# Kernel optimization log

Measured on AMD Instinct MI355X. Metric: run time of the kernel, lower is better.

Reference implementation:

```python
import jax, jax.numpy as jnp
import numpy as np

SCALING_FACTOR = 128.0


def setup_inputs() -> dict:
    key = jax.random.key(0)
    k1, k2, k3, k4 = jax.random.split(key, 4)
    B, G1, G2, DX, DZ, NT = 4, 128, 128, 2, 128, 2048
    x_grid = jax.random.uniform(k1, (B, G1, G2, DX), dtype=jnp.float32)
    z_grid = jax.random.normal(k2, (B, G1, G2, DZ), dtype=jnp.float32)
    xt = jax.random.uniform(k3, (B, NT, DX), dtype=jnp.float32)
    # raw (pre-softplus) lengthscale parameter, one per input dim
    init_ls = 0.1
    lengthscale_param = jnp.full((DX,), np.log(np.exp(init_ls) - 1.0), dtype=jnp.float32)
    lengthscale_param = lengthscale_param + 0.01 * jax.random.normal(k4, (DX,), dtype=jnp.float32)
    return {"x_grid": x_grid, "z_grid": z_grid, "xt": xt, "lengthscale_param": lengthscale_param}


def reference(x_grid, z_grid, xt, lengthscale_param):
    B = x_grid.shape[0]
    dx = x_grid.shape[-1]
    dz = z_grid.shape[-1]
    # flatten spatial grid dims -> (B, ng, d)
    xg = x_grid.reshape(B, -1, dx)
    zg = z_grid.reshape(B, -1, dz)
    # lengthscale = 1e-5 + softplus(param), shape (dx,)
    ls = 1e-5 + jax.nn.softplus(lengthscale_param)
    # pairwise scaled squared distances: (B, nt, ng)
    diff = (xt[:, :, None, :] - xg[:, None, :, :]) / ls  # (B, nt, ng, dx)
    dist2 = jnp.sum(diff * diff, axis=-1)
    weights = jnp.exp(-0.5 * dist2)  # (B, nt, ng)
    # weighted smoothing onto targets
    out = jnp.einsum("btg,bgz->btz", weights, zg) / SCALING_FACTOR
    return out
```

## Files before the change

kernel.cpp:

```cpp
#include <hip/hip_runtime.h>
#include <hip/hip_bf16.h>
#include <cstdint>
#include <cstddef>


typedef float  f32x4  __attribute__((ext_vector_type(4)));
typedef float  f32x16 __attribute__((ext_vector_type(16)));
typedef short  short8 __attribute__((ext_vector_type(8)));
typedef unsigned short ushort4v __attribute__((ext_vector_type(4)));
typedef unsigned short ushort8 __attribute__((ext_vector_type(8)));

#if __has_builtin(__builtin_amdgcn_exp2f)
#define EXP2F(x) __builtin_amdgcn_exp2f(x)
#else
#define EXP2F(x) exp2f(x)
#endif

#define AS1C(p) ((const __attribute__((address_space(1))) void*)(p))
#define AS3(p)  ((__attribute__((address_space(3))) void*)(p))

__device__ __forceinline__ unsigned short bf16_bits(float f) {
  __bf16 h = (__bf16)f;
  return __builtin_bit_cast(unsigned short, h);
}

__global__ __launch_bounds__(256) void pre_kernel(
    const float* __restrict__ x_grid, const float* __restrict__ z_grid,
    const float* __restrict__ xt, const float* __restrict__ lsp,
    unsigned short* __restrict__ zgb, float* __restrict__ xg_trip,
    float* __restrict__ xt4)
{
  __shared__ unsigned short lt[64 * 128];
  const int bid = blockIdx.x;
  const int b   = bid >> 8;
  const int grp = bid & 255;
  const int tid = threadIdx.x;
  const size_t gbase = (size_t)b * 16384 + grp * 64;
  const float sc = 1.0f / 128.0f;

  const float* zr = z_grid + gbase * 128;
  #pragma unroll
  for (int it = 0; it < 8; ++it) {
    const int idx = it * 256 + tid;
    const int row = idx >> 5, c4 = idx & 31;
    f32x4 v = *(const f32x4*)(zr + row * 128 + c4 * 4);
    ushort4v o;
    o.x = bf16_bits(v.x * sc); o.y = bf16_bits(v.y * sc);
    o.z = bf16_bits(v.z * sc); o.w = bf16_bits(v.w * sc);
    *(ushort4v*)(lt + row * 128 + c4 * 4) = o;
  }

  if (tid < 128) {
    const float ls0 = 1e-5f + log1pf(expf(lsp[0]));
    const float ls1 = 1e-5f + log1pf(expf(lsp[1]));
    const float cs  = sqrtf(0.7213475204444817f);
    const float s0 = cs / ls0, s1 = cs / ls1;
    if (tid < 64) {
      const size_t g = gbase + tid;
      const float u0 = x_grid[g * 2 + 0] * s0;
      const float u1 = x_grid[g * 2 + 1] * s1;
      float* d = xg_trip + g * 3;
      d[0] = 2.0f * u0; d[1] = 2.0f * u1; d[2] = -(u0 * u0 + u1 * u1);
    } else if (bid < 128) {
      const int bx = bid >> 5;
      const int r  = (bid & 31) * 64 + (tid - 64);
      const float u0 = xt[((size_t)(bx * 2048 + r)) * 2 + 0] * s0;
      const float u1 = xt[((size_t)(bx * 2048 + r)) * 2 + 1] * s1;
      f32x4 d; d.x = u0; d.y = u1; d.z = -(u0 * u0 + u1 * u1); d.w = 0.0f;
      *(f32x4*)(xt4 + ((size_t)(bx * 2048 + r)) * 4) = d;
    }
  }

  __syncthreads();

  const int q2p = tid >> 7, c = tid & 127;
  #pragma unroll
  for (int h = 0; h < 4; ++h) {
    ushort8 o;
    #pragma unroll
    for (int hi = 0; hi < 2; ++hi)
      #pragma unroll
      for (int j = 0; j < 4; ++j)
        o[hi * 4 + j] = lt[(h * 16 + 4 * q2p + 8 * hi + j) * 128 + c];
    *(ushort8*)(zgb + ((size_t)(b * 1024 + grp * 4 + h)) * 2048
                    + (size_t)(q2p * 128 + c) * 8) = o;
  }
}

__global__ __launch_bounds__(128, 2) void main_kernel(
    const unsigned short* __restrict__ zgb,
    const float* __restrict__ xg_trip,
    const float* __restrict__ xt4,
    float* __restrict__ out)
{
  __shared__ __align__(128) char smem[12288 + 12288];
  char* ring = smem;
  char* trip = smem + 12288;

  const int raw = blockIdx.x;
  const int lid = (raw & 7) * 128 + (raw >> 3);
  const int mt  = lid & 15;
  const int b   = (lid >> 4) & 3;
  const int ksp = lid >> 6;

  const int tid = threadIdx.x;
  const int rh  = tid >> 6;
  const int l   = tid & 63;
  const int l31 = l & 31;
  const int q2  = l >> 5;

  float at0[2], at1[2], ca[2];
  #pragma unroll
  for (int mi = 0; mi < 2; ++mi) {
    const int r = mt * 128 + rh * 64 + mi * 32 + l31;
    f32x4 v = *(const f32x4*)(xt4 + ((size_t)(b * 2048 + r)) * 4);
    at0[mi] = v.x; at1[mi] = v.y; ca[mi] = v.z;
  }

  f32x16 acc[2][4];
  #pragma unroll
  for (int mi = 0; mi < 2; ++mi)
    #pragma unroll
    for (int ni = 0; ni < 4; ++ni)
      #pragma unroll
      for (int e = 0; e < 16; ++e)
        acc[mi][ni][e] = 0.0f;

  const char* zsrc = (const char*)zgb + ((size_t)(b * 1024 + ksp * 64)) * 4096;
  const char* tsrc = (const char*)xg_trip + ((size_t)(b * 16384 + ksp * 1024)) * 12;

  auto stage = [&](int s) {
    const char* zs = zsrc + (size_t)s * 4096 + rh * 2048;
    char* zd = ring + (s % 3) * 4096 + rh * 2048;
    __builtin_amdgcn_global_load_lds(AS1C(zs + l * 16), AS3(zd + l * 16), 16, 0, 0);
    __builtin_amdgcn_global_load_lds(AS1C(zs + 1024 + l * 16),
                                     AS3(zd + 1024 + l * 16), 16, 0, 0);
  };

  #pragma unroll
  for (int w = 0; w < 6; ++w) {
    const int off = (rh * 6 + w) * 1024 + l * 16;
    __builtin_amdgcn_global_load_lds(AS1C(tsrc + off), AS3(trip + off), 16, 0, 0);
  }
  stage(0);
  stage(1);

  for (int s = 0; s < 64; ++s) {
    if (s < 63) { asm volatile("s_waitcnt vmcnt(2)" ::: "memory"); }
    else        { asm volatile("s_waitcnt vmcnt(0)" ::: "memory"); }
    __builtin_amdgcn_s_barrier();
    asm volatile("" ::: "memory");

    if (s + 2 < 64) stage(s + 2);

    const float* tb = (const float*)(trip + s * 192 + q2 * 48);
    f32x4 L0 = *(const f32x4*)(tb + 0);
    f32x4 L1 = *(const f32x4*)(tb + 4);
    f32x4 L2 = *(const f32x4*)(tb + 8);
    f32x4 H0 = *(const f32x4*)(tb + 24);
    f32x4 H1 = *(const f32x4*)(tb + 28);
    f32x4 H2 = *(const f32x4*)(tb + 32);
    float g0[8], g1[8], cb[8];
    g0[0]=L0.x; g1[0]=L0.y; cb[0]=L0.z;
    g0[1]=L0.w; g1[1]=L1.x; cb[1]=L1.y;
    g0[2]=L1.z; g1[2]=L1.w; cb[2]=L2.x;
    g0[3]=L2.y; g1[3]=L2.z; cb[3]=L2.w;
    g0[4]=H0.x; g1[4]=H0.y; cb[4]=H0.z;
    g0[5]=H0.w; g1[5]=H1.x; cb[5]=H1.y;
    g0[6]=H1.z; g1[6]=H1.w; cb[6]=H2.x;
    g0[7]=H2.y; g1[7]=H2.z; cb[7]=H2.w;

    const char* zt = ring + (s % 3) * 4096 + q2 * 2048 + l31 * 16;
    short8 bfr[4];
    #pragma unroll
    for (int ni = 0; ni < 4; ++ni)
      bfr[ni] = *(const short8*)(zt + ni * 512);

    short8 af[2];
    #pragma unroll
    for (int mi = 0; mi < 2; ++mi) {
      union { short8 s8; __bf16 e[8]; } u;
      #pragma unroll
      for (int j = 0; j < 8; ++j) {
        float arg = __builtin_fmaf(at0[mi], g0[j],
                    __builtin_fmaf(at1[mi], g1[j], ca[mi] + cb[j]));
        u.e[j] = (__bf16)EXP2F(arg);
      }
      af[mi] = u.s8;
    }

    #pragma unroll
    for (int mi = 0; mi < 2; ++mi)
      #pragma unroll
      for (int ni = 0; ni < 4; ++ni)
        acc[mi][ni] = __builtin_amdgcn_mfma_f32_32x32x16_bf16(
            af[mi], bfr[ni], acc[mi][ni], 0, 0, 0);
  }

  #pragma unroll
  for (int mi = 0; mi < 2; ++mi)
    #pragma unroll
    for (int ni = 0; ni < 4; ++ni)
      #pragma unroll
      for (int r = 0; r < 16; ++r) {
        const int row = mt * 128 + rh * 64 + mi * 32
                      + (r & 3) + 8 * (r >> 2) + 4 * q2;
        atomicAdd(out + ((size_t)b * 2048 + row) * 128 + ni * 32 + l31,
                  acc[mi][ni][r]);
      }
}

extern "C" void kernel_launch(void* const* d_in, const int* in_sizes, int n_in,
                              void* d_out, int out_size, void* d_ws, size_t ws_size,
                              hipStream_t stream) {
  const float* x_grid = (const float*)d_in[0];
  const float* z_grid = (const float*)d_in[1];
  const float* xt     = (const float*)d_in[2];
  const float* lsp    = (const float*)d_in[3];
  float* out = (float*)d_out;

  char* ws = (char*)d_ws;
  unsigned short* zgb = (unsigned short*)ws;
  float* xg_trip = (float*)(ws + 16777216);
  float* xt4     = (float*)(ws + 16777216 + 786432);

  hipMemsetAsync(d_out, 0, (size_t)out_size * sizeof(float), stream);
  pre_kernel<<<1024, 256, 0, stream>>>(x_grid, z_grid, xt, lsp,
                                       zgb, xg_trip, xt4);
  main_kernel<<<1024, 128, 0, stream>>>(zgb, xg_trip, xt4, out);
}
```

Baseline: 171.0 us.

## Split K across wave pairs with LDS reduction and replace atomics by partial-sum reduce

Each main_kernel block now has 256 threads: two wave pairs work on adjacent K chunks and combine their accumulators through LDS, which halves the grid to 512 blocks. When the workspace is large enough, the final per-K-split results go as plain stores into a partials buffer, and a new reduce_kernel sums the 8 splits. This replaces the memset plus fp32 atomics to the output. The cost is a larger 64KB LDS footprint per block, extra syncs, and a third kernel launch that reads 32MB of partials.

```diff
diff --git a/kernel.cpp b/kernel.cpp
--- a/kernel.cpp
+++ b/kernel.cpp
@@ -87,27 +87,31 @@
   }
 }
 
-__global__ __launch_bounds__(128, 2) void main_kernel(
+__global__ __launch_bounds__(256, 2) void main_kernel(
     const unsigned short* __restrict__ zgb,
     const float* __restrict__ xg_trip,
     const float* __restrict__ xt4,
-    float* __restrict__ out)
+    float* __restrict__ out,
+    float* __restrict__ partials)
 {
-  __shared__ __align__(128) char smem[12288 + 12288];
+  __shared__ __align__(128) char smem[65536];
   char* ring = smem;
-  char* trip = smem + 12288;
+  char* trip = smem + 24576;
 
   const int raw = blockIdx.x;
-  const int lid = (raw & 7) * 128 + (raw >> 3);
+  const int lid = (raw & 7) * 64 + (raw >> 3);
   const int mt  = lid & 15;
   const int b   = (lid >> 4) & 3;
   const int ksp = lid >> 6;
 
   const int tid = threadIdx.x;
-  const int rh  = tid >> 6;
+  const int wv  = tid >> 6;
   const int l   = tid & 63;
+  const int rh  = wv & 1;
+  const int kk  = wv >> 1;
   const int l31 = l & 31;
   const int q2  = l >> 5;
+  const int chunk = ksp * 2 + kk;
 
   float at0[2], at1[2], ca[2];
   #pragma unroll
@@ -126,12 +130,12 @@
       for (int e = 0; e < 16; ++e)
         acc[mi][ni][e] = 0.0f;
 
-  const char* zsrc = (const char*)zgb + ((size_t)(b * 1024 + ksp * 64)) * 4096;
-  const char* tsrc = (const char*)xg_trip + ((size_t)(b * 16384 + ksp * 1024)) * 12;
+  const char* zsrc = (const char*)zgb + ((size_t)(b * 1024 + chunk * 64)) * 4096;
+  const char* tsrc = (const char*)xg_trip + ((size_t)(b * 16384 + ksp * 2048)) * 12;
 
   auto stage = [&](int s) {
     const char* zs = zsrc + (size_t)s * 4096 + rh * 2048;
-    char* zd = ring + (s % 3) * 4096 + rh * 2048;
+    char* zd = ring + (s % 3) * 8192 + kk * 4096 + rh * 2048;
     __builtin_amdgcn_global_load_lds(AS1C(zs + l * 16), AS3(zd + l * 16), 16, 0, 0);
     __builtin_amdgcn_global_load_lds(AS1C(zs + 1024 + l * 16),
                                      AS3(zd + 1024 + l * 16), 16, 0, 0);
@@ -139,12 +143,13 @@
 
   #pragma unroll
   for (int w = 0; w < 6; ++w) {
-    const int off = (rh * 6 + w) * 1024 + l * 16;
+    const int off = wv * 6144 + w * 1024 + l * 16;
     __builtin_amdgcn_global_load_lds(AS1C(tsrc + off), AS3(trip + off), 16, 0, 0);
   }
   stage(0);
   stage(1);
 
+  #pragma unroll 3
   for (int s = 0; s < 64; ++s) {
     if (s < 63) { asm volatile("s_waitcnt vmcnt(2)" ::: "memory"); }
     else        { asm volatile("s_waitcnt vmcnt(0)" ::: "memory"); }
@@ -153,7 +158,7 @@
 
     if (s + 2 < 64) stage(s + 2);
 
-    const float* tb = (const float*)(trip + s * 192 + q2 * 48);
+    const float* tb = (const float*)(trip + kk * 12288 + s * 192 + q2 * 48);
     f32x4 L0 = *(const f32x4*)(tb + 0);
     f32x4 L1 = *(const f32x4*)(tb + 4);
     f32x4 L2 = *(const f32x4*)(tb + 8);
@@ -170,7 +175,7 @@
     g0[6]=H1.z; g1[6]=H1.w; cb[6]=H2.x;
     g0[7]=H2.y; g1[7]=H2.z; cb[7]=H2.w;
 
-    const char* zt = ring + (s % 3) * 4096 + q2 * 2048 + l31 * 16;
+    const char* zt = ring + (s % 3) * 8192 + kk * 4096 + q2 * 2048 + l31 * 16;
     short8 bfr[4];
     #pragma unroll
     for (int ni = 0; ni < 4; ++ni)
@@ -197,17 +202,63 @@
             af[mi], bfr[ni], acc[mi][ni], 0, 0, 0);
   }
 
-  #pragma unroll
-  for (int mi = 0; mi < 2; ++mi)
-    #pragma unroll
-    for (int ni = 0; ni < 4; ++ni)
-      #pragma unroll
-      for (int r = 0; r < 16; ++r) {
-        const int row = mt * 128 + rh * 64 + mi * 32
-                      + (r & 3) + 8 * (r >> 2) + 4 * q2;
-        atomicAdd(out + ((size_t)b * 2048 + row) * 128 + ni * 32 + l31,
-                  acc[mi][ni][r]);
+  __syncthreads();
+  if (kk == 1) {
+    #pragma unroll
+    for (int mi = 0; mi < 2; ++mi)
+      #pragma unroll
+      for (int ni = 0; ni < 4; ++ni)
+        #pragma unroll
+        for (int q = 0; q < 4; ++q) {
+          f32x4 v;
+          v.x = acc[mi][ni][q * 4 + 0]; v.y = acc[mi][ni][q * 4 + 1];
+          v.z = acc[mi][ni][q * 4 + 2]; v.w = acc[mi][ni][q * 4 + 3];
+          *(f32x4*)(smem + rh * 32768 + (mi * 4 + ni) * 4096 + q * 1024 + l * 16) = v;
+        }
+  }
+  __syncthreads();
+  if (kk == 0) {
+    float* pb = partials ? partials + ((size_t)(ksp * 64 + b * 16 + mt)) * 16384
+                         : nullptr;
+    #pragma unroll
+    for (int mi = 0; mi < 2; ++mi)
+      #pragma unroll
+      for (int ni = 0; ni < 4; ++ni) {
+        #pragma unroll
+        for (int q = 0; q < 4; ++q) {
+          f32x4 v = *(const f32x4*)(smem + rh * 32768 + (mi * 4 + ni) * 4096
+                                         + q * 1024 + l * 16);
+          acc[mi][ni][q * 4 + 0] += v.x; acc[mi][ni][q * 4 + 1] += v.y;
+          acc[mi][ni][q * 4 + 2] += v.z; acc[mi][ni][q * 4 + 3] += v.w;
+        }
+        #pragma unroll
+        for (int r = 0; r < 16; ++r) {
+          const int row = rh * 64 + mi * 32
+                        + (r & 3) + 8 * (r >> 2) + 4 * q2;
+          const int col = ni * 32 + l31;
+          if (pb) {
+            pb[row * 128 + col] = acc[mi][ni][r];
+          } else {
+            atomicAdd(out + ((size_t)b * 2048 + mt * 128 + row) * 128 + col,
+                      acc[mi][ni][r]);
+          }
+        }
       }
+  }
+}
+
+__global__ __launch_bounds__(256) void reduce_kernel(
+    const float* __restrict__ partials, float* __restrict__ out)
+{
+  const size_t base = ((size_t)blockIdx.x * 256 + threadIdx.x) * 4;
+  const float* p = partials + base;
+  f32x4 s = *(const f32x4*)p;
+  #pragma unroll
+  for (int ksv = 1; ksv < 8; ++ksv) {
+    f32x4 v = *(const f32x4*)(p + (size_t)ksv * 1048576);
+    s.x += v.x; s.y += v.y; s.z += v.z; s.w += v.w;
+  }
+  *(f32x4*)(out + base) = s;
 }
 
 extern "C" void kernel_launch(void* const* d_in, const int* in_sizes, int n_in,
@@ -223,9 +274,15 @@
   unsigned short* zgb = (unsigned short*)ws;
   float* xg_trip = (float*)(ws + 16777216);
   float* xt4     = (float*)(ws + 16777216 + 786432);
-
-  hipMemsetAsync(d_out, 0, (size_t)out_size * sizeof(float), stream);
+  const size_t poff = 16777216 + 786432 + 131072;
+  const bool use_partials = ws_size >= poff + 33554432;
+  float* partials = use_partials ? (float*)(ws + poff) : nullptr;
+
+  if (!use_partials)
+    hipMemsetAsync(d_out, 0, (size_t)out_size * sizeof(float), stream);
   pre_kernel<<<1024, 256, 0, stream>>>(x_grid, z_grid, xt, lsp,
                                        zgb, xg_trip, xt4);
-  main_kernel<<<1024, 128, 0, stream>>>(zgb, xg_trip, xt4, out);
-}
+  main_kernel<<<512, 256, 0, stream>>>(zgb, xg_trip, xt4, out, partials);
+  if (use_partials)
+    reduce_kernel<<<1024, 256, 0, stream>>>(partials, out);
+}
```

New measurement: 140.8 us. -17.7%, faster.

## Shrink main-kernel tiles, deepen pipeline, replace atomics with partial-sum reduction

Applied to the files above, without the earlier changes.

Each main-kernel block now covers 64 target rows instead of 128 and 8 K-splits instead of 16. Each warp holds a single 32-row MFMA tile, which cuts registers enough to raise the occupancy hint to 4 blocks per SIMD. The grid triplets are streamed through a 4-slot LDS ring with prefetch depth 3 instead of being preloaded, shrinking LDS use. When workspace allows, per-K-split results go to a partials buffer and a separate reduce kernel sums them, replacing the memset and float atomics. The trade-off is twice as many exp evaluations per B-fragment load, extra global traffic for the partials, and an added launch.

```diff
diff --git a/kernel.cpp b/kernel.cpp
--- a/kernel.cpp
+++ b/kernel.cpp
@@ -87,73 +87,71 @@
   }
 }
 
-__global__ __launch_bounds__(128, 2) void main_kernel(
+__global__ __launch_bounds__(128, 4) void main_kernel(
     const unsigned short* __restrict__ zgb,
     const float* __restrict__ xg_trip,
     const float* __restrict__ xt4,
-    float* __restrict__ out)
+    float* __restrict__ out,
+    float* __restrict__ partials)
 {
-  __shared__ __align__(128) char smem[12288 + 12288];
+  __shared__ __align__(128) char smem[4 * 4096 + 4 * 256];
   char* ring = smem;
-  char* trip = smem + 12288;
+  char* trg  = smem + 16384;
 
   const int raw = blockIdx.x;
   const int lid = (raw & 7) * 128 + (raw >> 3);
-  const int mt  = lid & 15;
-  const int b   = (lid >> 4) & 3;
-  const int ksp = lid >> 6;
+  const int mt  = lid & 31;
+  const int b   = (lid >> 5) & 3;
+  const int ksp = lid >> 7;
 
   const int tid = threadIdx.x;
-  const int rh  = tid >> 6;
+  const int w   = tid >> 6;
   const int l   = tid & 63;
   const int l31 = l & 31;
   const int q2  = l >> 5;
 
-  float at0[2], at1[2], ca[2];
-  #pragma unroll
-  for (int mi = 0; mi < 2; ++mi) {
-    const int r = mt * 128 + rh * 64 + mi * 32 + l31;
-    f32x4 v = *(const f32x4*)(xt4 + ((size_t)(b * 2048 + r)) * 4);
-    at0[mi] = v.x; at1[mi] = v.y; ca[mi] = v.z;
-  }
-
-  f32x16 acc[2][4];
-  #pragma unroll
-  for (int mi = 0; mi < 2; ++mi)
-    #pragma unroll
-    for (int ni = 0; ni < 4; ++ni)
-      #pragma unroll
-      for (int e = 0; e < 16; ++e)
-        acc[mi][ni][e] = 0.0f;
-
-  const char* zsrc = (const char*)zgb + ((size_t)(b * 1024 + ksp * 64)) * 4096;
-  const char* tsrc = (const char*)xg_trip + ((size_t)(b * 16384 + ksp * 1024)) * 12;
+  const int r = mt * 64 + w * 32 + l31;
+  f32x4 tv = *(const f32x4*)(xt4 + ((size_t)(b * 2048 + r)) * 4);
+  const float at0 = tv.x, at1 = tv.y, ca = tv.z;
+
+  f32x16 acc[4];
+  #pragma unroll
+  for (int ni = 0; ni < 4; ++ni)
+    #pragma unroll
+    for (int e = 0; e < 16; ++e)
+      acc[ni][e] = 0.0f;
+
+  const char* zsrc = (const char*)zgb + ((size_t)(b * 1024 + ksp * 128)) * 4096;
+  const char* tsrc = (const char*)xg_trip + ((size_t)(b * 16384 + ksp * 2048)) * 12;
 
   auto stage = [&](int s) {
-    const char* zs = zsrc + (size_t)s * 4096 + rh * 2048;
-    char* zd = ring + (s % 3) * 4096 + rh * 2048;
+    const int sl = s & 3;
+    const char* zs = zsrc + (size_t)s * 4096 + w * 2048;
+    char* zd = ring + sl * 4096 + w * 2048;
     __builtin_amdgcn_global_load_lds(AS1C(zs + l * 16), AS3(zd + l * 16), 16, 0, 0);
     __builtin_amdgcn_global_load_lds(AS1C(zs + 1024 + l * 16),
                                      AS3(zd + 1024 + l * 16), 16, 0, 0);
+    if (l < 6) {
+      __builtin_amdgcn_global_load_lds(
+          AS1C(tsrc + (size_t)s * 192 + w * 96 + l * 16),
+          AS3(trg + sl * 256 + w * 96 + l * 16), 16, 0, 0);
+    }
   };
 
-  #pragma unroll
-  for (int w = 0; w < 6; ++w) {
-    const int off = (rh * 6 + w) * 1024 + l * 16;
-    __builtin_amdgcn_global_load_lds(AS1C(tsrc + off), AS3(trip + off), 16, 0, 0);
-  }
   stage(0);
   stage(1);
-
-  for (int s = 0; s < 64; ++s) {
-    if (s < 63) { asm volatile("s_waitcnt vmcnt(2)" ::: "memory"); }
-    else        { asm volatile("s_waitcnt vmcnt(0)" ::: "memory"); }
+  stage(2);
+
+  #pragma unroll 4
+  for (int s = 0; s < 128; ++s) {
+    if (s < 126) { asm volatile("s_waitcnt vmcnt(6)" ::: "memory"); }
+    else         { asm volatile("s_waitcnt vmcnt(0)" ::: "memory"); }
     __builtin_amdgcn_s_barrier();
     asm volatile("" ::: "memory");
 
-    if (s + 2 < 64) stage(s + 2);
-
-    const float* tb = (const float*)(trip + s * 192 + q2 * 48);
+    if (s + 3 < 128) stage(s + 3);
+
+    const float* tb = (const float*)(trg + (s & 3) * 256 + q2 * 48);
     f32x4 L0 = *(const f32x4*)(tb + 0);
     f32x4 L1 = *(const f32x4*)(tb + 4);
     f32x4 L2 = *(const f32x4*)(tb + 8);
@@ -170,44 +168,57 @@
     g0[6]=H1.z; g1[6]=H1.w; cb[6]=H2.x;
     g0[7]=H2.y; g1[7]=H2.z; cb[7]=H2.w;
 
-    const char* zt = ring + (s % 3) * 4096 + q2 * 2048 + l31 * 16;
-    short8 bfr[4];
-    #pragma unroll
-    for (int ni = 0; ni < 4; ++ni)
-      bfr[ni] = *(const short8*)(zt + ni * 512);
-
-    short8 af[2];
-    #pragma unroll
-    for (int mi = 0; mi < 2; ++mi) {
-      union { short8 s8; __bf16 e[8]; } u;
-      #pragma unroll
-      for (int j = 0; j < 8; ++j) {
-        float arg = __builtin_fmaf(at0[mi], g0[j],
-                    __builtin_fmaf(at1[mi], g1[j], ca[mi] + cb[j]));
-        u.e[j] = (__bf16)EXP2F(arg);
-      }
-      af[mi] = u.s8;
-    }
-
-    #pragma unroll
-    for (int mi = 0; mi < 2; ++mi)
-      #pragma unroll
-      for (int ni = 0; ni < 4; ++ni)
-        acc[mi][ni] = __builtin_amdgcn_mfma_f32_32x32x16_bf16(
-            af[mi], bfr[ni], acc[mi][ni], 0, 0, 0);
-  }
-
-  #pragma unroll
-  for (int mi = 0; mi < 2; ++mi)
+    union { short8 s8; __bf16 e[8]; } u;
+    #pragma unroll
+    for (int j = 0; j < 8; ++j) {
+      float arg = __builtin_fmaf(at0, g0[j],
+                  __builtin_fmaf(at1, g1[j], ca + cb[j]));
+      u.e[j] = (__bf16)EXP2F(arg);
+    }
+    const short8 af = u.s8;
+
+    const char* zt = ring + (s & 3) * 4096 + q2 * 2048 + l31 * 16;
+    #pragma unroll
+    for (int ni = 0; ni < 4; ++ni) {
+      short8 bfr = *(const short8*)(zt + ni * 512);
+      acc[ni] = __builtin_amdgcn_mfma_f32_32x32x16_bf16(af, bfr, acc[ni], 0, 0, 0);
+    }
+  }
+
+  if (partials) {
+    float* pb = partials + (size_t)ksp * 1048576
+              + ((size_t)(b * 2048 + mt * 64 + w * 32)) * 128;
     #pragma unroll
     for (int ni = 0; ni < 4; ++ni)
       #pragma unroll
-      for (int r = 0; r < 16; ++r) {
-        const int row = mt * 128 + rh * 64 + mi * 32
-                      + (r & 3) + 8 * (r >> 2) + 4 * q2;
+      for (int rr = 0; rr < 16; ++rr) {
+        const int row = (rr & 3) + 8 * (rr >> 2) + 4 * q2;
+        pb[row * 128 + ni * 32 + l31] = acc[ni][rr];
+      }
+  } else {
+    #pragma unroll
+    for (int ni = 0; ni < 4; ++ni)
+      #pragma unroll
+      for (int rr = 0; rr < 16; ++rr) {
+        const int row = mt * 64 + w * 32 + (rr & 3) + 8 * (rr >> 2) + 4 * q2;
         atomicAdd(out + ((size_t)b * 2048 + row) * 128 + ni * 32 + l31,
-                  acc[mi][ni][r]);
+                  acc[ni][rr]);
       }
+  }
+}
+
+__global__ __launch_bounds__(256) void reduce_kernel(
+    const float* __restrict__ partials, float* __restrict__ out)
+{
+  const size_t base = ((size_t)blockIdx.x * 256 + threadIdx.x) * 4;
+  const float* p = partials + base;
+  f32x4 s = *(const f32x4*)p;
+  #pragma unroll
+  for (int ksv = 1; ksv < 8; ++ksv) {
+    f32x4 v = *(const f32x4*)(p + (size_t)ksv * 1048576);
+    s.x += v.x; s.y += v.y; s.z += v.z; s.w += v.w;
+  }
+  *(f32x4*)(out + base) = s;
 }
 
 extern "C" void kernel_launch(void* const* d_in, const int* in_sizes, int n_in,
@@ -223,9 +234,15 @@
   unsigned short* zgb = (unsigned short*)ws;
   float* xg_trip = (float*)(ws + 16777216);
   float* xt4     = (float*)(ws + 16777216 + 786432);
-
-  hipMemsetAsync(d_out, 0, (size_t)out_size * sizeof(float), stream);
+  const size_t poff = 16777216 + 786432 + 131072;
+  const bool use_partials = ws_size >= poff + 33554432;
+  float* partials = use_partials ? (float*)(ws + poff) : nullptr;
+
+  if (!use_partials)
+    hipMemsetAsync(d_out, 0, (size_t)out_size * sizeof(float), stream);
   pre_kernel<<<1024, 256, 0, stream>>>(x_grid, z_grid, xt, lsp,
                                        zgb, xg_trip, xt4);
-  main_kernel<<<1024, 128, 0, stream>>>(zgb, xg_trip, xt4, out);
-}
+  main_kernel<<<1024, 128, 0, stream>>>(zgb, xg_trip, xt4, out, partials);
+  if (use_partials)
+    reduce_kernel<<<1024, 256, 0, stream>>>(partials, out);
+}
```

Measured after the change: 149.0 us. 12.8% less time.
